# Kernel optimization log

Hardware: AMD Instinct MI355X
Metric: run time of the kernel (lower is better)

## Reference

```python
import jax, jax.numpy as jnp
import numpy as np

N_NODES = 28


def _gcn_norm(edge_index, n):
    """PyG GCNConv normalization: add self-loops, sym-normalize by deg^-1/2."""
    loops = jnp.arange(n, dtype=edge_index.dtype)
    src = jnp.concatenate([edge_index[0], loops])
    dst = jnp.concatenate([edge_index[1], loops])
    ones = jnp.ones(src.shape[0], dtype=jnp.float32)
    deg = jax.ops.segment_sum(ones, dst, num_segments=n)  # in-degree incl. self-loop
    dinv = jnp.where(deg > 0, 1.0 / jnp.sqrt(deg), 0.0)
    norm = dinv[src] * dinv[dst]  # [E+N]
    return src, dst, norm


def _gcn_conv(x, W, b, src, dst, norm, n):
    # x: [B, N, Cin] -> [B, N, Cout]; linear first, then normalized scatter-add.
    h = jnp.einsum('bni,io->bno', x, W)
    msg = h[:, src, :] * norm[None, :, None]          # gather + edge scaling
    out = jnp.zeros_like(h).at[:, dst, :].add(msg)     # scatter-add over dst
    return out + b


def setup_inputs() -> dict:
    key = jax.random.key(0)
    k1, k2, k3, k4 = jax.random.split(key, 4)
    B, N, E, H = 65536, N_NODES, 756, 64
    x = jax.random.normal(k1, (B, N), dtype=jnp.float32)
    edge_index = jax.random.randint(k2, (2, E), 0, N, dtype=jnp.int64)
    W1 = jax.random.normal(k3, (1, H), dtype=jnp.float32) * (1.0 / np.sqrt(1.0))
    b1 = jnp.zeros((H,), dtype=jnp.float32)
    W2 = jax.random.normal(k4, (H, 1), dtype=jnp.float32) * (1.0 / np.sqrt(H))
    b2 = jnp.zeros((1,), dtype=jnp.float32)
    return {"x": x, "edge_index": edge_index, "W1": W1, "b1": b1, "W2": W2, "b2": b2}


def reference(x, edge_index, W1, b1, W2, b2):
    n = x.shape[1]
    src, dst, norm = _gcn_norm(edge_index, n)
    h = x[:, :, None]                                  # [B, N, 1] node features
    h = jax.nn.relu(_gcn_conv(h, W1, b1, src, dst, norm, n))
    # dropout(0.2) is identity in eval mode
    h = _gcn_conv(h, W2, b2, src, dst, norm, n)        # [B, N, 1]
    return h[:, :, 0]
```

## Files before the change

### kernel.cpp

```cpp
#include <hip/hip_runtime.h>
#include <math.h>

#define NN 28
#define NH 64

__global__ __launch_bounds__(256) void gcn_fused_kernel(
    const float* __restrict__ x, const int* __restrict__ ei, int E,
    const float* __restrict__ W1, const float* __restrict__ b1,
    const float* __restrict__ W2, const float* __restrict__ b2,
    float* __restrict__ out, int B) {
  __shared__ __align__(16) float A[NN * NN];
  __shared__ float dinv[NN];
  __shared__ float cpos_s, cneg_s;
  __shared__ int flag_s;
  const int t = threadIdx.x;

  if (t < NN) dinv[t] = 1.0f;
  for (int i = t; i < NN * NN; i += 256) A[i] = 0.0f;
  if (t == 0) { cpos_s = 0.0f; cneg_s = 0.0f; flag_s = 0; }
  __syncthreads();

  for (int e = t; e < E; e += 256) atomicAdd(&dinv[ei[E + e]], 1.0f);
  __syncthreads();
  if (t < NN) dinv[t] = 1.0f / sqrtf(dinv[t]);
  __syncthreads();

  for (int e = t; e < E; e += 256) {
    int s = ei[e];
    int d = ei[E + e];
    atomicAdd(&A[d * NN + s], dinv[s] * dinv[d]);
  }
  if (t < NN) atomicAdd(&A[t * NN + t], dinv[t] * dinv[t]);

  if (t < NH) {
    float w1 = W1[t], w2 = W2[t];
    if (w1 > 0.0f)      atomicAdd(&cpos_s, w1 * w2);
    else if (w1 < 0.0f) atomicAdd(&cneg_s, w1 * w2);
    if (b1[t] != 0.0f) atomicOr(&flag_s, 1);
  }
  __syncthreads();

  const int b = blockIdx.x * 256 + t;
  if (b >= B) return;

  const float4* xp = (const float4*)(x + (size_t)b * NN);
  float xv[NN];
#pragma unroll
  for (int k = 0; k < 7; ++k) {
    float4 v = xp[k];
    xv[4 * k + 0] = v.x; xv[4 * k + 1] = v.y;
    xv[4 * k + 2] = v.z; xv[4 * k + 3] = v.w;
  }

  const float4* A4 = (const float4*)A;

  float s[NN];
#pragma unroll
  for (int n = 0; n < NN; ++n) {
    float acc = 0.0f;
#pragma unroll
    for (int k = 0; k < 7; ++k) {
      float4 a = A4[n * 7 + k];
      acc = fmaf(a.x, xv[4 * k + 0], acc);
      acc = fmaf(a.y, xv[4 * k + 1], acc);
      acc = fmaf(a.z, xv[4 * k + 2], acc);
      acc = fmaf(a.w, xv[4 * k + 3], acc);
    }
    s[n] = acc;
  }

  const float cpos = cpos_s;
  const float cneg = cneg_s;
  const bool  fast = (flag_s == 0);

  float z[NN];
  if (fast) {
#pragma unroll
    for (int n = 0; n < NN; ++n)
      z[n] = s[n] * (s[n] > 0.0f ? cpos : cneg);
  } else {
#pragma unroll
    for (int n = 0; n < NN; ++n) z[n] = 0.0f;
    for (int o = 0; o < NH; ++o) {
      float w1 = W1[o], bb = b1[o], w2 = W2[o];
#pragma unroll
      for (int n = 0; n < NN; ++n)
        z[n] = fmaf(fmaxf(fmaf(s[n], w1, bb), 0.0f), w2, z[n]);
    }
  }

  const float bias2 = b2[0];
  float ov[NN];
#pragma unroll
  for (int n = 0; n < NN; ++n) {
    float acc = bias2;
#pragma unroll
    for (int k = 0; k < 7; ++k) {
      float4 a = A4[n * 7 + k];
      acc = fmaf(a.x, z[4 * k + 0], acc);
      acc = fmaf(a.y, z[4 * k + 1], acc);
      acc = fmaf(a.z, z[4 * k + 2], acc);
      acc = fmaf(a.w, z[4 * k + 3], acc);
    }
    ov[n] = acc;
  }

  float4* op = (float4*)(out + (size_t)b * NN);
#pragma unroll
  for (int k = 0; k < 7; ++k) {
    float4 v;
    v.x = ov[4 * k + 0]; v.y = ov[4 * k + 1];
    v.z = ov[4 * k + 2]; v.w = ov[4 * k + 3];
    op[k] = v;
  }
}

extern "C" void kernel_launch(void* const* d_in, const int* in_sizes, int n_in,
                              void* d_out, int out_size, void* d_ws, size_t ws_size,
                              hipStream_t stream) {
  const float* x  = (const float*)d_in[0];
  const int*   ei = (const int*)d_in[1];
  const float* W1 = (const float*)d_in[2];
  const float* b1 = (const float*)d_in[3];
  const float* W2 = (const float*)d_in[4];
  const float* b2 = (const float*)d_in[5];
  float* out = (float*)d_out;

  const int E = in_sizes[1] / 2;
  const int B = in_sizes[0] / NN;

  const int threads = 256;
  const int blocks = (B + threads - 1) / threads;
  gcn_fused_kernel<<<blocks, threads, 0, stream>>>(x, ei, E, W1, b1, W2, b2,
                                                   out, B);
}
```

Measured before the change: 83.14 us.

## Split each batch element's rows across two threads and coalesce output via LDS

```diff
diff --git a/kernel.cpp b/kernel.cpp
--- a/kernel.cpp
+++ b/kernel.cpp
@@ -1,10 +1,13 @@
 #include <hip/hip_runtime.h>
 #include <math.h>
 
-#define NN 28
-#define NH 64
+#define NN  28
+#define NH  64
+#define EPB 256
+#define TPB 512
+#define LSTR 29
 
-__global__ __launch_bounds__(256) void gcn_fused_kernel(
+__global__ __launch_bounds__(TPB, 2) void gcn_fused_kernel(
     const float* __restrict__ x, const int* __restrict__ ei, int E,
     const float* __restrict__ W1, const float* __restrict__ b1,
     const float* __restrict__ W2, const float* __restrict__ b2,
@@ -13,19 +16,21 @@
   __shared__ float dinv[NN];
   __shared__ float cpos_s, cneg_s;
   __shared__ int flag_s;
+  __shared__ float xchg[EPB * LSTR];
+
   const int t = threadIdx.x;
 
   if (t < NN) dinv[t] = 1.0f;
-  for (int i = t; i < NN * NN; i += 256) A[i] = 0.0f;
+  for (int i = t; i < NN * NN; i += TPB) A[i] = 0.0f;
   if (t == 0) { cpos_s = 0.0f; cneg_s = 0.0f; flag_s = 0; }
   __syncthreads();
 
-  for (int e = t; e < E; e += 256) atomicAdd(&dinv[ei[E + e]], 1.0f);
+  for (int e = t; e < E; e += TPB) atomicAdd(&dinv[ei[E + e]], 1.0f);
   __syncthreads();
   if (t < NN) dinv[t] = 1.0f / sqrtf(dinv[t]);
   __syncthreads();
 
-  for (int e = t; e < E; e += 256) {
+  for (int e = t; e < E; e += TPB) {
     int s = ei[e];
     int d = ei[E + e];
     atomicAdd(&A[d * NN + s], dinv[s] * dinv[d]);
@@ -40,78 +45,101 @@
   }
   __syncthreads();
 
-  const int b = blockIdx.x * 256 + t;
-  if (b >= B) return;
+  const int elem = t & (EPB - 1);
+  const int role = t >> 8;
+  const int row0 = role * 14;
+  const int b = blockIdx.x * EPB + elem;
+  const bool valid = (b < B);
 
-  const float4* xp = (const float4*)(x + (size_t)b * NN);
   float xv[NN];
+  if (valid) {
+    const float4* xp = (const float4*)(x + (size_t)b * NN);
 #pragma unroll
-  for (int k = 0; k < 7; ++k) {
-    float4 v = xp[k];
-    xv[4 * k + 0] = v.x; xv[4 * k + 1] = v.y;
-    xv[4 * k + 2] = v.z; xv[4 * k + 3] = v.w;
+    for (int k = 0; k < 7; ++k) {
+      float4 v = xp[k];
+      xv[4 * k + 0] = v.x; xv[4 * k + 1] = v.y;
+      xv[4 * k + 2] = v.z; xv[4 * k + 3] = v.w;
+    }
+  } else {
+#pragma unroll
+    for (int m = 0; m < NN; ++m) xv[m] = 0.0f;
   }
 
   const float4* A4 = (const float4*)A;
 
-  float s[NN];
+  float s14[14];
 #pragma unroll
-  for (int n = 0; n < NN; ++n) {
-    float acc = 0.0f;
+  for (int i = 0; i < 14; ++i) {
+    const int n = row0 + i;
+    float a0 = 0.0f, a1 = 0.0f;
 #pragma unroll
     for (int k = 0; k < 7; ++k) {
       float4 a = A4[n * 7 + k];
-      acc = fmaf(a.x, xv[4 * k + 0], acc);
-      acc = fmaf(a.y, xv[4 * k + 1], acc);
-      acc = fmaf(a.z, xv[4 * k + 2], acc);
-      acc = fmaf(a.w, xv[4 * k + 3], acc);
+      a0 = fmaf(a.x, xv[4 * k + 0], a0);
+      a1 = fmaf(a.y, xv[4 * k + 1], a1);
+      a0 = fmaf(a.z, xv[4 * k + 2], a0);
+      a1 = fmaf(a.w, xv[4 * k + 3], a1);
     }
-    s[n] = acc;
+    s14[i] = a0 + a1;
   }
 
   const float cpos = cpos_s;
   const float cneg = cneg_s;
-  const bool  fast = (flag_s == 0);
-
-  float z[NN];
-  if (fast) {
+  float z14[14];
+  if (flag_s == 0) {
 #pragma unroll
-    for (int n = 0; n < NN; ++n)
-      z[n] = s[n] * (s[n] > 0.0f ? cpos : cneg);
+    for (int i = 0; i < 14; ++i)
+      z14[i] = s14[i] * (s14[i] > 0.0f ? cpos : cneg);
   } else {
 #pragma unroll
-    for (int n = 0; n < NN; ++n) z[n] = 0.0f;
+    for (int i = 0; i < 14; ++i) z14[i] = 0.0f;
     for (int o = 0; o < NH; ++o) {
       float w1 = W1[o], bb = b1[o], w2 = W2[o];
 #pragma unroll
-      for (int n = 0; n < NN; ++n)
-        z[n] = fmaf(fmaxf(fmaf(s[n], w1, bb), 0.0f), w2, z[n]);
+      for (int i = 0; i < 14; ++i)
+        z14[i] = fmaf(fmaxf(fmaf(s14[i], w1, bb), 0.0f), w2, z14[i]);
     }
   }
 
+#pragma unroll
+  for (int i = 0; i < 14; ++i) xchg[elem * LSTR + row0 + i] = z14[i];
+  __syncthreads();
+
+  float zv[NN];
+#pragma unroll
+  for (int j = 0; j < NN; ++j) zv[j] = xchg[elem * LSTR + j];
+
   const float bias2 = b2[0];
-  float ov[NN];
+  float o14[14];
 #pragma unroll
-  for (int n = 0; n < NN; ++n) {
-    float acc = bias2;
+  for (int i = 0; i < 14; ++i) {
+    const int n = row0 + i;
+    float a0 = bias2, a1 = 0.0f;
 #pragma unroll
     for (int k = 0; k < 7; ++k) {
       float4 a = A4[n * 7 + k];
-      acc = fmaf(a.x, z[4 * k + 0], acc);
-      acc = fmaf(a.y, z[4 * k + 1], acc);
-      acc = fmaf(a.z, z[4 * k + 2], acc);
-      acc = fmaf(a.w, z[4 * k + 3], acc);
+      a0 = fmaf(a.x, zv[4 * k + 0], a0);
+      a1 = fmaf(a.y, zv[4 * k + 1], a1);
+      a0 = fmaf(a.z, zv[4 * k + 2], a0);
+      a1 = fmaf(a.w, zv[4 * k + 3], a1);
     }
-    ov[n] = acc;
+    o14[i] = a0 + a1;
   }
 
-  float4* op = (float4*)(out + (size_t)b * NN);
+  __syncthreads();
 #pragma unroll
-  for (int k = 0; k < 7; ++k) {
-    float4 v;
-    v.x = ov[4 * k + 0]; v.y = ov[4 * k + 1];
-    v.z = ov[4 * k + 2]; v.w = ov[4 * k + 3];
-    op[k] = v;
+  for (int i = 0; i < 14; ++i) xchg[elem * LSTR + row0 + i] = o14[i];
+  __syncthreads();
+
+  const size_t blk_base = (size_t)blockIdx.x * (EPB * NN);
+  const size_t total = (size_t)B * NN;
+#pragma unroll
+  for (int k = 0; k < 14; ++k) {
+    unsigned g = (unsigned)t + (unsigned)k * TPB;
+    unsigned e = g / NN;
+    unsigned j = g - e * NN;
+    size_t gi = blk_base + g;
+    if (gi < total) out[gi] = xchg[e * LSTR + j];
   }
 }
 
@@ -129,8 +157,6 @@
   const int E = in_sizes[1] / 2;
   const int B = in_sizes[0] / NN;
 
-  const int threads = 256;
-  const int blocks = (B + threads - 1) / threads;
-  gcn_fused_kernel<<<blocks, threads, 0, stream>>>(x, ei, E, W1, b1, W2, b2,
-                                                   out, B);
+  const int blocks = (B + EPB - 1) / EPB;
+  gcn_fused_kernel<<<blocks, TPB, 0, stream>>>(x, ei, E, W1, b1, W2, b2, out, B);
 }
```

Measured after the change: 77.27 us. -7.1%, faster.

## Compute both graph aggregations with split-bf16 MFMA and per-wave LDS transpose

Applied to the files above, without the earlier changes.

```diff
diff --git a/kernel.cpp b/kernel.cpp
--- a/kernel.cpp
+++ b/kernel.cpp
@@ -1,10 +1,27 @@
 #include <hip/hip_runtime.h>
 #include <math.h>
 
-#define NN 28
-#define NH 64
+#define NN   28
+#define NH   64
+#define WAVES 8
+#define TPB  (WAVES * 64)
+#define EPW  16
+#define EPB  (WAVES * EPW)
+#define ZSTR 29
 
-__global__ __launch_bounds__(256) void gcn_fused_kernel(
+typedef __attribute__((ext_vector_type(8))) short bf16x8;
+typedef __attribute__((ext_vector_type(4))) float f32x4;
+
+static __device__ __forceinline__ short f2bf(float f) {
+  unsigned u = __float_as_uint(f);
+  u = (u + 0x7FFFu + ((u >> 16) & 1u)) >> 16;
+  return (short)u;
+}
+static __device__ __forceinline__ float bf2f(short h) {
+  return __uint_as_float(((unsigned)(unsigned short)h) << 16);
+}
+
+__global__ __launch_bounds__(TPB) void gcn_mfma_kernel(
     const float* __restrict__ x, const int* __restrict__ ei, int E,
     const float* __restrict__ W1, const float* __restrict__ b1,
     const float* __restrict__ W2, const float* __restrict__ b2,
@@ -13,19 +30,33 @@
   __shared__ float dinv[NN];
   __shared__ float cpos_s, cneg_s;
   __shared__ int flag_s;
+  __shared__ float zbuf[WAVES][EPW * ZSTR];
+
   const int t = threadIdx.x;
+  const int wave = t >> 6, lane = t & 63;
+  const int q = lane >> 4, l15 = lane & 15;
+
+  const int gelem0 = (blockIdx.x * WAVES + wave) * EPW;
+  const int me = gelem0 + l15;
+  const bool mv = (me < B);
+  const float* xr = x + (size_t)(mv ? me : 0) * NN + q * 8;
+  float4 xv0 = *(const float4*)xr;
+  float4 xv1;
+  if (q < 3) xv1 = *(const float4*)(xr + 4);
+  else       xv1 = make_float4(0.f, 0.f, 0.f, 0.f);
+  if (!mv) { xv0 = make_float4(0.f,0.f,0.f,0.f); xv1 = make_float4(0.f,0.f,0.f,0.f); }
 
   if (t < NN) dinv[t] = 1.0f;
-  for (int i = t; i < NN * NN; i += 256) A[i] = 0.0f;
+  for (int i = t; i < NN * NN; i += TPB) A[i] = 0.0f;
   if (t == 0) { cpos_s = 0.0f; cneg_s = 0.0f; flag_s = 0; }
   __syncthreads();
 
-  for (int e = t; e < E; e += 256) atomicAdd(&dinv[ei[E + e]], 1.0f);
+  for (int e = t; e < E; e += TPB) atomicAdd(&dinv[ei[E + e]], 1.0f);
   __syncthreads();
   if (t < NN) dinv[t] = 1.0f / sqrtf(dinv[t]);
   __syncthreads();
 
-  for (int e = t; e < E; e += 256) {
+  for (int e = t; e < E; e += TPB) {
     int s = ei[e];
     int d = ei[E + e];
     atomicAdd(&A[d * NN + s], dinv[s] * dinv[d]);
@@ -40,78 +71,104 @@
   }
   __syncthreads();
 
-  const int b = blockIdx.x * 256 + t;
-  if (b >= B) return;
-
-  const float4* xp = (const float4*)(x + (size_t)b * NN);
-  float xv[NN];
+  bf16x8 bhi0, bhi1, blo0, blo1;
+  {
+    const int n0 = l15, n1 = 16 + l15;
 #pragma unroll
-  for (int k = 0; k < 7; ++k) {
-    float4 v = xp[k];
-    xv[4 * k + 0] = v.x; xv[4 * k + 1] = v.y;
-    xv[4 * k + 2] = v.z; xv[4 * k + 3] = v.w;
+    for (int j = 0; j < 8; ++j) {
+      const int k = q * 8 + j;
+      float a0 = (k < NN) ? A[n0 * NN + k] : 0.0f;
+      float a1 = (n1 < NN && k < NN) ? A[n1 * NN + k] : 0.0f;
+      short h0 = f2bf(a0), h1 = f2bf(a1);
+      bhi0[j] = h0; blo0[j] = f2bf(a0 - bf2f(h0));
+      bhi1[j] = h1; blo1[j] = f2bf(a1 - bf2f(h1));
+    }
   }
 
-  const float4* A4 = (const float4*)A;
-
-  float s[NN];
+  bf16x8 xhi, xlo;
+  {
+    float xf[8] = {xv0.x, xv0.y, xv0.z, xv0.w, xv1.x, xv1.y, xv1.z, xv1.w};
 #pragma unroll
-  for (int n = 0; n < NN; ++n) {
-    float acc = 0.0f;
-#pragma unroll
-    for (int k = 0; k < 7; ++k) {
-      float4 a = A4[n * 7 + k];
-      acc = fmaf(a.x, xv[4 * k + 0], acc);
-      acc = fmaf(a.y, xv[4 * k + 1], acc);
-      acc = fmaf(a.z, xv[4 * k + 2], acc);
-      acc = fmaf(a.w, xv[4 * k + 3], acc);
+    for (int j = 0; j < 8; ++j) {
+      short h = f2bf(xf[j]);
+      xhi[j] = h; xlo[j] = f2bf(xf[j] - bf2f(h));
     }
-    s[n] = acc;
   }
 
-  const float cpos = cpos_s;
-  const float cneg = cneg_s;
-  const bool  fast = (flag_s == 0);
+  f32x4 acc0 = {0.f, 0.f, 0.f, 0.f}, acc1 = {0.f, 0.f, 0.f, 0.f};
+  acc0 = __builtin_amdgcn_mfma_f32_16x16x32_bf16(xhi, bhi0, acc0, 0, 0, 0);
+  acc0 = __builtin_amdgcn_mfma_f32_16x16x32_bf16(xlo, bhi0, acc0, 0, 0, 0);
+  acc0 = __builtin_amdgcn_mfma_f32_16x16x32_bf16(xhi, blo0, acc0, 0, 0, 0);
+  acc1 = __builtin_amdgcn_mfma_f32_16x16x32_bf16(xhi, bhi1, acc1, 0, 0, 0);
+  acc1 = __builtin_amdgcn_mfma_f32_16x16x32_bf16(xlo, bhi1, acc1, 0, 0, 0);
+  acc1 = __builtin_amdgcn_mfma_f32_16x16x32_bf16(xhi, blo1, acc1, 0, 0, 0);
 
-  float z[NN];
-  if (fast) {
+  const float cpos = cpos_s, cneg = cneg_s;
+  float z0[4], z1[4];
+  if (flag_s == 0) {
 #pragma unroll
-    for (int n = 0; n < NN; ++n)
-      z[n] = s[n] * (s[n] > 0.0f ? cpos : cneg);
+    for (int r = 0; r < 4; ++r) {
+      z0[r] = acc0[r] * (acc0[r] > 0.0f ? cpos : cneg);
+      z1[r] = acc1[r] * (acc1[r] > 0.0f ? cpos : cneg);
+    }
   } else {
 #pragma unroll
-    for (int n = 0; n < NN; ++n) z[n] = 0.0f;
+    for (int r = 0; r < 4; ++r) { z0[r] = 0.0f; z1[r] = 0.0f; }
     for (int o = 0; o < NH; ++o) {
       float w1 = W1[o], bb = b1[o], w2 = W2[o];
 #pragma unroll
-      for (int n = 0; n < NN; ++n)
-        z[n] = fmaf(fmaxf(fmaf(s[n], w1, bb), 0.0f), w2, z[n]);
+      for (int r = 0; r < 4; ++r) {
+        z0[r] = fmaf(fmaxf(fmaf(acc0[r], w1, bb), 0.0f), w2, z0[r]);
+        z1[r] = fmaf(fmaxf(fmaf(acc1[r], w1, bb), 0.0f), w2, z1[r]);
+      }
     }
   }
 
+  float* zb = zbuf[wave];
+#pragma unroll
+  for (int r = 0; r < 4; ++r) {
+    const int m = q * 4 + r;
+    zb[m * ZSTR + l15] = z0[r];
+    if (l15 < NN - 16) zb[m * ZSTR + 16 + l15] = z1[r];
+  }
+  __builtin_amdgcn_wave_barrier();
+
+  bf16x8 zhi, zlo;
+#pragma unroll
+  for (int j = 0; j < 8; ++j) {
+    const int k = q * 8 + j;
+    float v = (k < NN) ? zb[l15 * ZSTR + k] : 0.0f;
+    short h = f2bf(v);
+    zhi[j] = h; zlo[j] = f2bf(v - bf2f(h));
+  }
+  __builtin_amdgcn_wave_barrier();
+
+  f32x4 occ0 = {0.f, 0.f, 0.f, 0.f}, occ1 = {0.f, 0.f, 0.f, 0.f};
+  occ0 = __builtin_amdgcn_mfma_f32_16x16x32_bf16(zhi, bhi0, occ0, 0, 0, 0);
+  occ0 = __builtin_amdgcn_mfma_f32_16x16x32_bf16(zlo, bhi0, occ0, 0, 0, 0);
+  occ0 = __builtin_amdgcn_mfma_f32_16x16x32_bf16(zhi, blo0, occ0, 0, 0, 0);
+  occ1 = __builtin_amdgcn_mfma_f32_16x16x32_bf16(zhi, bhi1, occ1, 0, 0, 0);
+  occ1 = __builtin_amdgcn_mfma_f32_16x16x32_bf16(zlo, bhi1, occ1, 0, 0, 0);
+  occ1 = __builtin_amdgcn_mfma_f32_16x16x32_bf16(zhi, blo1, occ1, 0, 0, 0);
+
   const float bias2 = b2[0];
-  float ov[NN];
 #pragma unroll
-  for (int n = 0; n < NN; ++n) {
-    float acc = bias2;
+  for (int r = 0; r < 4; ++r) {
+    const int m = q * 4 + r;
+    zb[m * ZSTR + l15] = occ0[r] + bias2;
+    if (l15 < NN - 16) zb[m * ZSTR + 16 + l15] = occ1[r] + bias2;
+  }
+  __builtin_amdgcn_wave_barrier();
+
+  const size_t obase = (size_t)gelem0 * NN;
+  const size_t total = (size_t)B * NN;
 #pragma unroll
-    for (int k = 0; k < 7; ++k) {
-      float4 a = A4[n * 7 + k];
-      acc = fmaf(a.x, z[4 * k + 0], acc);
-      acc = fmaf(a.y, z[4 * k + 1], acc);
-      acc = fmaf(a.z, z[4 * k + 2], acc);
-      acc = fmaf(a.w, z[4 * k + 3], acc);
-    }
-    ov[n] = acc;
-  }
-
-  float4* op = (float4*)(out + (size_t)b * NN);
-#pragma unroll
-  for (int k = 0; k < 7; ++k) {
-    float4 v;
-    v.x = ov[4 * k + 0]; v.y = ov[4 * k + 1];
-    v.z = ov[4 * k + 2]; v.w = ov[4 * k + 3];
-    op[k] = v;
+  for (int k7 = 0; k7 < 7; ++k7) {
+    const int flat = lane + 64 * k7;
+    const unsigned e = (unsigned)flat / NN;
+    const unsigned n = (unsigned)flat - e * NN;
+    if (obase + flat < total)
+      out[obase + flat] = zb[e * ZSTR + n];
   }
 }
 
@@ -129,8 +186,6 @@
   const int E = in_sizes[1] / 2;
   const int B = in_sizes[0] / NN;
 
-  const int threads = 256;
-  const int blocks = (B + threads - 1) / threads;
-  gcn_fused_kernel<<<blocks, threads, 0, stream>>>(x, ei, E, W1, b1, W2, b2,
-                                                   out, B);
+  const int blocks = (B + EPB - 1) / EPB;
+  gcn_mfma_kernel<<<blocks, TPB, 0, stream>>>(x, ei, E, W1, b1, W2, b2, out, B);
 }
```

Measured after the change: 75.15 us. 9.6% less time.
